# Kernel tuning notes

Measured on AMD Instinct MI355X. Metric: run time of the kernel, lower is better.

Reference implementation:

```python
import jax, jax.numpy as jnp
import numpy as np

N = 100000      # nodes
E = 1600000     # edges (before self loops)
IN_C, HID_C, OUT_C = 128, 64, 40


def setup_inputs() -> dict:
    key = jax.random.key(0)
    k = jax.random.split(key, 6)
    x = jax.random.normal(k[0], (N, IN_C), dtype=jnp.float32)
    edge_index = jax.random.randint(k[1], (2, E), 0, N, dtype=jnp.int64)
    W1 = jax.random.normal(k[2], (IN_C, HID_C), dtype=jnp.float32) * (1.0 / np.sqrt(IN_C))
    b1 = jnp.zeros((HID_C,), jnp.float32)
    W2 = jax.random.normal(k[3], (HID_C, OUT_C), dtype=jnp.float32) * (1.0 / np.sqrt(HID_C))
    b2 = jnp.zeros((OUT_C,), jnp.float32)
    beta2 = jnp.ones((), jnp.float32)  # learnable beta of prop2 (init 1.0)
    return {"x": x, "edge_index": edge_index, "W1": W1, "b1": b1,
            "W2": W2, "b2": b2, "beta2": beta2}


def _agnn_prop(x, src, dst, beta, n):
    # L2-normalize node features (F.normalize, eps=1e-12 on norm)
    xn = x * jax.lax.rsqrt(jnp.maximum(jnp.sum(x * x, axis=-1, keepdims=True), 1e-24))
    # per-edge cosine similarity scaled by beta
    alpha = beta * jnp.sum(xn[src] * xn[dst], axis=-1)           # [E']
    # scatter-softmax over edges grouped by destination node
    amax = jax.ops.segment_max(alpha, dst, num_segments=n)       # [N]
    e = jnp.exp(alpha - amax[dst])
    denom = jax.ops.segment_sum(e, dst, num_segments=n)          # [N]
    w = e / denom[dst]                                           # [E']
    # gather-weighted aggregation of (unnormalized) source features
    return jax.ops.segment_sum(x[src] * w[:, None], dst, num_segments=n)


def reference(x, edge_index, W1, b1, W2, b2, beta2):
    n = x.shape[0]
    # AGNNConv add_self_loops=True
    loops = jnp.arange(n, dtype=edge_index.dtype)
    src = jnp.concatenate([edge_index[0], loops])
    dst = jnp.concatenate([edge_index[1], loops])
    h = jax.nn.relu(x @ W1 + b1)                                 # [N, HID]
    h = _agnn_prop(h, src, dst, jnp.float32(1.0), n)             # prop1: fixed beta=1
    h = _agnn_prop(h, src, dst, beta2, n)                        # prop2: learnable beta
    logits = h @ W2 + b2                                         # [N, OUT]
    return jax.nn.log_softmax(logits, axis=1)
```

## Files before the change

### kernel.cpp

```cpp
#include <hip/hip_runtime.h>
#include <math.h>

#define INC 128
#define HID 64
#define OUTC 40
#define SHIFT 9
#define MAXB 256
#define NPB 64
#define ONB 96
#define LSW 41
#define SRCM 0x1FFFF
#define PLDS 12288

typedef _Float16 half2_t __attribute__((ext_vector_type(2)));

__device__ inline void fma4(float4& a, float s, const float4& w) {
    a.x += s * w.x; a.y += s * w.y; a.z += s * w.z; a.w += s * w.w;
}
__device__ inline unsigned pkh(float a, float b) {
    unsigned short ua = __builtin_bit_cast(unsigned short, (_Float16)a);
    unsigned short ub = __builtin_bit_cast(unsigned short, (_Float16)b);
    return (unsigned)ua | ((unsigned)ub << 16);
}
__device__ inline float fdot2_(unsigned a, unsigned b, float c) {
#if __has_builtin(__builtin_amdgcn_fdot2)
    return __builtin_amdgcn_fdot2(__builtin_bit_cast(half2_t, a),
                                  __builtin_bit_cast(half2_t, b), c, false);
#else
    half2_t ha = __builtin_bit_cast(half2_t, a);
    half2_t hb = __builtin_bit_cast(half2_t, b);
    return fmaf((float)ha[0], (float)hb[0], fmaf((float)ha[1], (float)hb[1], c));
#endif
}
__device__ inline float dot4(const uint4& a, const uint4& b) {
    float d = fdot2_(a.x, b.x, 0.f);
    d = fdot2_(a.y, b.y, d);
    d = fdot2_(a.z, b.z, d);
    d = fdot2_(a.w, b.w, d);
    return d;
}
__device__ inline void accum8(float* acc, float s, const uint4& a) {
    half2_t p;
    p = __builtin_bit_cast(half2_t, a.x); acc[0] += s * (float)p[0]; acc[1] += s * (float)p[1];
    p = __builtin_bit_cast(half2_t, a.y); acc[2] += s * (float)p[0]; acc[3] += s * (float)p[1];
    p = __builtin_bit_cast(half2_t, a.z); acc[4] += s * (float)p[0]; acc[5] += s * (float)p[1];
    p = __builtin_bit_cast(half2_t, a.w); acc[6] += s * (float)p[0]; acc[7] += s * (float)p[1];
}
__device__ inline void unpack8(float* f, const uint4& a) {
    half2_t p;
    p = __builtin_bit_cast(half2_t, a.x); f[0] = (float)p[0]; f[1] = (float)p[1];
    p = __builtin_bit_cast(half2_t, a.y); f[2] = (float)p[0]; f[3] = (float)p[1];
    p = __builtin_bit_cast(half2_t, a.z); f[4] = (float)p[0]; f[5] = (float)p[1];
    p = __builtin_bit_cast(half2_t, a.w); f[6] = (float)p[0]; f[7] = (float)p[1];
}
__device__ inline void dacc4(float4& a, unsigned xp_, const uint4& w) {
    a.x = fdot2_(xp_, w.x, a.x);
    a.y = fdot2_(xp_, w.y, a.y);
    a.z = fdot2_(xp_, w.z, a.z);
    a.w = fdot2_(xp_, w.w, a.w);
}
template<int CTRL>
__device__ inline float dppadd(float d) {
    int x = __builtin_amdgcn_update_dpp(0, __builtin_bit_cast(int, d),
                                        CTRL, 0xf, 0xf, true);
    return d + __builtin_bit_cast(float, x);
}
__device__ inline float red8(float d) {
    d = dppadd<0xB1>(d);
    d = dppadd<0x4E>(d);
    d = dppadd<0x141>(d);
    return d;
}
__device__ inline float red16(float d) {
    d = dppadd<0xB1>(d);
    d = dppadd<0x4E>(d);
    d = dppadd<0x141>(d);
    d = dppadd<0x140>(d);
    return d;
}
#define EXP2(x) __builtin_amdgcn_exp2f(x)


__global__ __launch_bounds__(256) void k_hist(const int* __restrict__ ei, int E,
                                              int* __restrict__ bucket_cnt,
                                              int* __restrict__ blk_cnt, int nbuck) {
    __shared__ int lh[MAXB];
    int tid = threadIdx.x;
    for (int i = tid; i < nbuck; i += 256) lh[i] = 0;
    __syncthreads();
    int base = blockIdx.x * 4096;
    int end = min(base + 4096, E);
    for (int e = base + tid; e < end; e += 256)
        atomicAdd(&lh[ei[E + e] >> SHIFT], 1);
    __syncthreads();
    for (int i = tid; i < nbuck; i += 256) {
        int v = lh[i];
        blk_cnt[blockIdx.x * MAXB + i] = v;
        if (v) atomicAdd(&bucket_cnt[i], v);
    }
}

__global__ __launch_bounds__(256) void k_bscan(const int* __restrict__ bucket_cnt,
                                               int* __restrict__ pair_base,
                                               int* __restrict__ pair_fill,
                                               int* __restrict__ row_ptr,
                                               int n, int E, int nbuck) {
    __shared__ int tmp[MAXB];
    int tid = threadIdx.x;
    int cnt = (tid < nbuck) ? bucket_cnt[tid] : 0;
    tmp[tid] = cnt;
    __syncthreads();
    for (int off = 1; off < 256; off <<= 1) {
        int t = (tid >= off) ? tmp[tid - off] : 0;
        __syncthreads();
        tmp[tid] += t;
        __syncthreads();
    }
    if (tid < nbuck) { int pb = tmp[tid] - cnt; pair_base[tid] = pb; pair_fill[tid] = pb; }
    if (tid == 0) row_ptr[n] = E;
}

__global__ __launch_bounds__(256) void k_bin(const int* __restrict__ ei, int E,
                                             const int* __restrict__ blk_cnt,
                                             int* __restrict__ pair_fill,
                                             unsigned* __restrict__ pairs, int nbuck) {
    __shared__ int lbase[MAXB];
    int tid = threadIdx.x;
    for (int i = tid; i < nbuck; i += 256) {
        int v = blk_cnt[blockIdx.x * MAXB + i];
        lbase[i] = v ? atomicAdd(&pair_fill[i], v) : 0;
    }
    __syncthreads();
    int base = blockIdx.x * 4096;
    int end = min(base + 4096, E);
    for (int e = base + tid; e < end; e += 256) {
        int s = ei[e], d = ei[E + e];
        int pos = atomicAdd(&lbase[d >> SHIFT], 1);
        pairs[pos] = (unsigned)s | ((unsigned)(d & ((1 << SHIFT) - 1)) << 17);
    }
}

__global__ __launch_bounds__(256) void k_build(const unsigned* __restrict__ pairs,
                                               const int* __restrict__ pair_base,
                                               const int* __restrict__ bucket_cnt,
                                               int* __restrict__ row_ptr,
                                               int* __restrict__ csr_src, int n) {
    __shared__ int cnt[1 << SHIFT];
    __shared__ int offs[1 << SHIFT];
    __shared__ int stmp[256];
    __shared__ unsigned plds[PLDS];
    int b = blockIdx.x;
    int tid = threadIdx.x;
    int nb0 = b << SHIFT;
    int W = min(n - nb0, 1 << SHIFT);
    int p0 = pair_base[b], pc = bucket_cnt[b];
    bool inl = (pc <= PLDS);

    cnt[tid] = 0; cnt[tid + 256] = 0;
    if (inl) for (int i = tid; i < pc; i += 256) plds[i] = pairs[p0 + i];
    __syncthreads();
    if (inl) {
        for (int i = tid; i < pc; i += 256) atomicAdd(&cnt[plds[i] >> 17], 1);
    } else {
        for (int i = tid; i < pc; i += 256) atomicAdd(&cnt[pairs[p0 + i] >> 17], 1);
    }
    __syncthreads();

    int i0 = 2 * tid, i1 = 2 * tid + 1;
    int s0 = (i0 < W) ? cnt[i0] : 0;
    int s1 = (i1 < W) ? cnt[i1] : 0;
    int ps = s0 + s1;
    stmp[tid] = ps;
    __syncthreads();
    for (int off = 1; off < 256; off <<= 1) {
        int t = (tid >= off) ? stmp[tid - off] : 0;
        __syncthreads();
        stmp[tid] += t;
        __syncthreads();
    }
    int excl = stmp[tid] - ps;
    if (i0 < W) { row_ptr[nb0 + i0] = p0 + excl;      offs[i0] = excl; }
    if (i1 < W) { row_ptr[nb0 + i1] = p0 + excl + s0; offs[i1] = excl + s0; }
    __syncthreads();
    if (inl) {
        for (int i = tid; i < pc; i += 256) {
            unsigned pr = plds[i];
            int pos = atomicAdd(&offs[pr >> 17], 1);
            csr_src[p0 + pos] = (int)(pr & SRCM);
        }
    } else {
        for (int i = tid; i < pc; i += 256) {
            unsigned pr = pairs[p0 + i];
            int pos = atomicAdd(&offs[pr >> 17], 1);
            csr_src[p0 + pos] = (int)(pr & SRCM);
        }
    }
}


__global__ __launch_bounds__(256, 4) void k_linear1(const float* __restrict__ x,
                                                    const float* __restrict__ W1,
                                                    const float* __restrict__ b1,
                                                    uint2* __restrict__ X1,
                                                    float* __restrict__ nrm1, int n) {
    __shared__ unsigned Wp[64 * 64];
    __shared__ unsigned xp[64 * 64];
    int tid = threadIdx.x;
    int base = blockIdx.x * NPB;

    for (int t = tid; t < 1024; t += 256) {
        int kp = t >> 4;
        int c4 = t & 15;
        float4 a = ((const float4*)W1)[(2 * kp) * 16 + c4];
        float4 b = ((const float4*)W1)[(2 * kp + 1) * 16 + c4];
        uint4 w;
        w.x = pkh(a.x, b.x); w.y = pkh(a.y, b.y);
        w.z = pkh(a.z, b.z); w.w = pkh(a.w, b.w);
        *(uint4*)&Wp[kp * 64 + c4 * 4] = w;
    }
    for (int t = tid; t < 1024; t += 256) {
        int nl = t >> 4;
        int k8 = t & 15;
        int gn = base + nl;
        float4 a, b;
        if (gn < n) {
            a = ((const float4*)x)[(size_t)gn * 32 + k8 * 2];
            b = ((const float4*)x)[(size_t)gn * 32 + k8 * 2 + 1];
        } else { a = make_float4(0,0,0,0); b = a; }
        uint4 v;
        v.x = pkh(a.x, a.y); v.y = pkh(a.z, a.w);
        v.z = pkh(b.x, b.y); v.w = pkh(b.z, b.w);
        int key = ((nl >> 2) & 3) << 2;
        *(uint4*)&xp[nl * 64 + ((k8 * 4) ^ key)] = v;
    }
    __syncthreads();

    int cg = tid & 15;
    int ng = tid >> 4;
    int n0 = ng * 4;
    const int key = (ng & 3) << 2;
    float4 acc0 = {0,0,0,0}, acc1 = {0,0,0,0}, acc2 = {0,0,0,0}, acc3 = {0,0,0,0};

    #pragma unroll 4
    for (int k4 = 0; k4 < 64; k4 += 4) {
        uint4 xq0 = *(uint4*)&xp[(n0 + 0) * 64 + (k4 ^ key)];
        uint4 xq1 = *(uint4*)&xp[(n0 + 1) * 64 + (k4 ^ key)];
        uint4 xq2 = *(uint4*)&xp[(n0 + 2) * 64 + (k4 ^ key)];
        uint4 xq3 = *(uint4*)&xp[(n0 + 3) * 64 + (k4 ^ key)];
        uint4 wq0 = *(uint4*)&Wp[(k4 + 0) * 64 + cg * 4];
        uint4 wq1 = *(uint4*)&Wp[(k4 + 1) * 64 + cg * 4];
        uint4 wq2 = *(uint4*)&Wp[(k4 + 2) * 64 + cg * 4];
        uint4 wq3 = *(uint4*)&Wp[(k4 + 3) * 64 + cg * 4];
        dacc4(acc0, xq0.x, wq0); dacc4(acc0, xq0.y, wq1); dacc4(acc0, xq0.z, wq2); dacc4(acc0, xq0.w, wq3);
        dacc4(acc1, xq1.x, wq0); dacc4(acc1, xq1.y, wq1); dacc4(acc1, xq1.z, wq2); dacc4(acc1, xq1.w, wq3);
        dacc4(acc2, xq2.x, wq0); dacc4(acc2, xq2.y, wq1); dacc4(acc2, xq2.z, wq2); dacc4(acc2, xq2.w, wq3);
        dacc4(acc3, xq3.x, wq0); dacc4(acc3, xq3.y, wq1); dacc4(acc3, xq3.z, wq2); dacc4(acc3, xq3.w, wq3);
    }

    float4 bb = ((const float4*)b1)[cg];
    float4 r[4] = {acc0, acc1, acc2, acc3};
    #pragma unroll
    for (int nl = 0; nl < 4; ++nl) {
        int node = base + n0 + nl;
        float4 v = r[nl];
        v.x = fmaxf(v.x + bb.x, 0.f); v.y = fmaxf(v.y + bb.y, 0.f);
        v.z = fmaxf(v.z + bb.z, 0.f); v.w = fmaxf(v.w + bb.w, 0.f);
        float q = v.x * v.x + v.y * v.y + v.z * v.z + v.w * v.w;
        q = red16(q);
        float rq = rsqrtf(fmaxf(q, 1e-24f));
        if (node < n) {
            X1[(size_t)node * 16 + cg] = make_uint2(pkh(v.x * rq, v.y * rq),
                                                    pkh(v.z * rq, v.w * rq));
            if (cg == 0) nrm1[node] = sqrtf(fmaxf(q, 1e-24f));
        }
    }
}


template<bool HFOUT>
__global__ __launch_bounds__(256) void k_prop(const uint4* __restrict__ X,
                                              const float* __restrict__ nrm,
                                              const int* __restrict__ row_ptr,
                                              const int* __restrict__ csr_src,
                                              const float* __restrict__ beta_ptr,
                                              uint4* __restrict__ Xout,
                                              float* __restrict__ nrm_out,
                                              float4* __restrict__ outf, int n) {
    int node = blockIdx.x * 4 + (threadIdx.x >> 6);
    if (node >= n) return;
    int lane = threadIdx.x & 63;
    int g = lane >> 3, gl = lane & 7;
    float beta = beta_ptr ? beta_ptr[0] : 1.0f;
    float b2 = beta * 1.4426950408889634f;

    uint4 hdp = X[(size_t)node * 8 + gl];
    float hdf[8]; unpack8(hdf, hdp);
    int s0 = row_ptr[node], s1 = row_ptr[node + 1];

    float ds = red8(dot4(hdp, hdp));
    float eself = EXP2(b2 * ds);
    float nd = nrm[node];
    float den0 = (g == 0) ? eself : 0.f;
    float es = (g == 0) ? eself * nd : 0.f;
    float acc[8];
    #pragma unroll
    for (int c = 0; c < 8; ++c) acc[c] = es * hdf[c];
    float den1 = 0.f;

    int j = s0;
    for (; j + 16 <= s1; j += 16) {
        int i0 = csr_src[j + g];
        int i1 = csr_src[j + 8 + g];
        uint4 a0 = X[(size_t)i0 * 8 + gl];
        uint4 a1 = X[(size_t)i1 * 8 + gl];
        float n0 = nrm[i0], n1 = nrm[i1];
        float d0 = red8(dot4(a0, hdp));
        float d1 = red8(dot4(a1, hdp));
        float e0 = EXP2(b2 * d0);
        float e1 = EXP2(b2 * d1);
        den0 += e0; den1 += e1;
        accum8(acc, e0 * n0, a0);
        accum8(acc, e1 * n1, a1);
    }
    for (; j < s1; j += 8) {
        int p0 = j + g;
        bool v0 = p0 < s1;
        int i0 = v0 ? csr_src[p0] : 0;
        uint4 a0 = X[(size_t)i0 * 8 + gl];
        float n0 = nrm[i0];
        float d0 = red8(dot4(a0, hdp));
        float e0 = v0 ? EXP2(b2 * d0) : 0.f;
        den0 += e0;
        accum8(acc, e0 * n0, a0);
    }

    float den = den0 + den1;
    #pragma unroll
    for (int c = 0; c < 8; ++c) {
        acc[c] += __shfl_xor(acc[c], 8, 64);
        acc[c] += __shfl_xor(acc[c], 16, 64);
        acc[c] += __shfl_xor(acc[c], 32, 64);
    }
    den += __shfl_xor(den, 8, 64);
    den += __shfl_xor(den, 16, 64);
    den += __shfl_xor(den, 32, 64);
    float inv = 1.0f / den;
    float o[8];
    #pragma unroll
    for (int c = 0; c < 8; ++c) o[c] = acc[c] * inv;

    if (HFOUT) {
        float q = 0.f;
        #pragma unroll
        for (int c = 0; c < 8; ++c) q += o[c] * o[c];
        q = red8(q);
        float rq = rsqrtf(fmaxf(q, 1e-24f));
        if (g == 0) {
            uint4 w;
            w.x = pkh(o[0] * rq, o[1] * rq);
            w.y = pkh(o[2] * rq, o[3] * rq);
            w.z = pkh(o[4] * rq, o[5] * rq);
            w.w = pkh(o[6] * rq, o[7] * rq);
            Xout[(size_t)node * 8 + gl] = w;
            if (gl == 0) nrm_out[node] = sqrtf(fmaxf(q, 1e-24f));
        }
    } else {
        if (g == 0) {
            outf[(size_t)node * 16 + gl * 2]     = make_float4(o[0], o[1], o[2], o[3]);
            outf[(size_t)node * 16 + gl * 2 + 1] = make_float4(o[4], o[5], o[6], o[7]);
        }
    }
}


__global__ __launch_bounds__(256) void k_out(const float* __restrict__ h,
                                             const float* __restrict__ W2,
                                             const float* __restrict__ b2,
                                             float* __restrict__ out, int n) {
    __shared__ float hs[ONB * HID];
    __shared__ float W2s[HID * OUTC];
    __shared__ float ls[ONB * LSW];
    int tid = threadIdx.x;
    int base = blockIdx.x * ONB;

    for (int i = tid; i < HID * OUTC / 4; i += 256)
        ((float4*)W2s)[i] = ((const float4*)W2)[i];
    for (int i = tid; i < ONB * 16; i += 256) {
        int nl = i >> 4, k4 = i & 15;
        int gn = base + nl;
        float4 v = (gn < n) ? ((const float4*)h)[(size_t)gn * 16 + k4]
                            : make_float4(0.f, 0.f, 0.f, 0.f);
        int swk = (k4 * 4) ^ (((nl >> 2) & 7) << 2);
        *(float4*)&hs[nl * HID + swk] = v;
    }
    __syncthreads();

    if (tid < 240) {
        int ng = tid / 10, cg = tid % 10;
        int n0 = ng * 4;
        const int sw = ((ng & 7) << 2);
        float4 acc0 = {0,0,0,0}, acc1 = {0,0,0,0}, acc2 = {0,0,0,0}, acc3 = {0,0,0,0};
        #pragma unroll 4
        for (int k = 0; k < HID; k += 4) {
            float4 w0 = *(float4*)&W2s[(k + 0) * OUTC + cg * 4];
            float4 w1 = *(float4*)&W2s[(k + 1) * OUTC + cg * 4];
            float4 w2 = *(float4*)&W2s[(k + 2) * OUTC + cg * 4];
            float4 w3 = *(float4*)&W2s[(k + 3) * OUTC + cg * 4];
            float4 x0 = *(float4*)&hs[(n0 + 0) * HID + (k ^ sw)];
            float4 x1 = *(float4*)&hs[(n0 + 1) * HID + (k ^ sw)];
            float4 x2 = *(float4*)&hs[(n0 + 2) * HID + (k ^ sw)];
            float4 x3 = *(float4*)&hs[(n0 + 3) * HID + (k ^ sw)];
            fma4(acc0, x0.x, w0); fma4(acc0, x0.y, w1); fma4(acc0, x0.z, w2); fma4(acc0, x0.w, w3);
            fma4(acc1, x1.x, w0); fma4(acc1, x1.y, w1); fma4(acc1, x1.z, w2); fma4(acc1, x1.w, w3);
            fma4(acc2, x2.x, w0); fma4(acc2, x2.y, w1); fma4(acc2, x2.z, w2); fma4(acc2, x2.w, w3);
            fma4(acc3, x3.x, w0); fma4(acc3, x3.y, w1); fma4(acc3, x3.z, w2); fma4(acc3, x3.w, w3);
        }
        float4 bb = ((const float4*)b2)[cg];
        float4 rr[4] = {acc0, acc1, acc2, acc3};
        #pragma unroll
        for (int i = 0; i < 4; ++i) {
            int lb = (n0 + i) * LSW + cg * 4;
            ls[lb + 0] = rr[i].x + bb.x;
            ls[lb + 1] = rr[i].y + bb.y;
            ls[lb + 2] = rr[i].z + bb.z;
            ls[lb + 3] = rr[i].w + bb.w;
        }
    }
    __syncthreads();

    if (tid < ONB) {
        int node = base + tid;
        if (node < n) {
            float m = -INFINITY;
            #pragma unroll
            for (int c = 0; c < OUTC; ++c) m = fmaxf(m, ls[tid * LSW + c]);
            float z = 0.f;
            #pragma unroll
            for (int c = 0; c < OUTC; ++c) z += __expf(ls[tid * LSW + c] - m);
            float lz = m + __logf(z);
            #pragma unroll
            for (int c = 0; c < OUTC; ++c)
                out[(size_t)node * OUTC + c] = ls[tid * LSW + c] - lz;
        }
    }
}


extern "C" void kernel_launch(void* const* d_in, const int* in_sizes, int n_in,
                              void* d_out, int out_size, void* d_ws, size_t ws_size,
                              hipStream_t stream) {
    const float* x   = (const float*)d_in[0];
    const int*   ei  = (const int*)d_in[1];
    const float* W1  = (const float*)d_in[2];
    const float* b1  = (const float*)d_in[3];
    const float* W2  = (const float*)d_in[4];
    const float* b2  = (const float*)d_in[5];
    const float* beta2 = (const float*)d_in[6];
    float* out = (float*)d_out;

    const int n = in_sizes[0] / INC;
    const int E = in_sizes[1] / 2;
    const int nbuck = (n + (1 << SHIFT) - 1) >> SHIFT;
    const int cgrid = (E + 4095) / 4096;

    char* p = (char*)d_ws;
    uint4* X1 = (uint4*)p;             p += (size_t)n * 8 * 16;
    uint4* X2 = (uint4*)p;             p += (size_t)n * 8 * 16;
    float* h3 = (float*)p;             p += (size_t)n * HID * 4;
    float* nrm1 = (float*)p;           p += (size_t)n * 4;
    float* nrm2 = (float*)p;           p += (size_t)n * 4;
    int* bucket_cnt  = (int*)p;        p += MAXB * 4;
    int* pair_base   = (int*)p;        p += MAXB * 4;
    int* pair_fill   = (int*)p;        p += MAXB * 4;
    int* row_ptr = (int*)p;            p += (size_t)(n + 1) * 4;
    int* csr_src = (int*)p;            p += (size_t)E * 4;
    int* blk_cnt = (int*)p;            p += (size_t)cgrid * MAXB * 4;
    unsigned* pairs = (unsigned*)h3;

    hipMemsetAsync(bucket_cnt, 0, MAXB * 4, stream);
    k_hist<<<cgrid, 256, 0, stream>>>(ei, E, bucket_cnt, blk_cnt, nbuck);
    k_bscan<<<1, 256, 0, stream>>>(bucket_cnt, pair_base, pair_fill, row_ptr, n, E, nbuck);
    k_bin<<<cgrid, 256, 0, stream>>>(ei, E, blk_cnt, pair_fill, pairs, nbuck);
    k_build<<<nbuck, 256, 0, stream>>>(pairs, pair_base, bucket_cnt, row_ptr, csr_src, n);

    k_linear1<<<(n + NPB - 1) / NPB, 256, 0, stream>>>(x, W1, b1, (uint2*)X1, nrm1, n);
    int pgrid = (n + 3) / 4;
    k_prop<true><<<pgrid, 256, 0, stream>>>(X1, nrm1, row_ptr, csr_src, nullptr,
                                            X2, nrm2, nullptr, n);
    k_prop<false><<<pgrid, 256, 0, stream>>>(X2, nrm2, row_ptr, csr_src, beta2,
                                             nullptr, nullptr, (float4*)h3, n);
    k_out<<<(n + ONB - 1) / ONB, 256, 0, stream>>>(h3, W2, b2, out, n);
}
```

Measured before the change: 195.2 us.

## Software-pipeline neighbor gathers in prop and store final prop output as fp16

The edge loop in k_prop is restructured into a single 16-wide loop that prefetches the next batch of neighbor indices, features and norms while computing the current one, with clamped indices and validity masks replacing the separate tail loop. The self-loop term is computed in closed form (exp2(beta) for a unit vector) instead of a dot product. The second propagation now writes fp16-packed features, which k_out unpacks, halving that intermediate's traffic. The risks are extra register pressure from the prefetch, redundant clamped loads in partial batches, and fp16 rounding of the unnormalized output before the final linear layer.

Result: faster. 190.5 us (-2.4%).

```diff
diff --git a/kernel.cpp b/kernel.cpp
--- a/kernel.cpp
+++ b/kernel.cpp
@@ -284,8 +284,7 @@
                                               const int* __restrict__ csr_src,
                                               const float* __restrict__ beta_ptr,
                                               uint4* __restrict__ Xout,
-                                              float* __restrict__ nrm_out,
-                                              float4* __restrict__ outf, int n) {
+                                              float* __restrict__ nrm_out, int n) {
     int node = blockIdx.x * 4 + (threadIdx.x >> 6);
     if (node >= n) return;
     int lane = threadIdx.x & 63;
@@ -294,44 +293,47 @@
     float b2 = beta * 1.4426950408889634f;
 
     uint4 hdp = X[(size_t)node * 8 + gl];
-    float hdf[8]; unpack8(hdf, hdp);
     int s0 = row_ptr[node], s1 = row_ptr[node + 1];
-
-    float ds = red8(dot4(hdp, hdp));
-    float eself = EXP2(b2 * ds);
     float nd = nrm[node];
+
+    float eself = (nd > 1.5e-12f) ? EXP2(b2) : 1.0f;
     float den0 = (g == 0) ? eself : 0.f;
     float es = (g == 0) ? eself * nd : 0.f;
-    float acc[8];
-    #pragma unroll
-    for (int c = 0; c < 8; ++c) acc[c] = es * hdf[c];
+    float acc[8] = {0, 0, 0, 0, 0, 0, 0, 0};
+    accum8(acc, es, hdp);
     float den1 = 0.f;
 
-    int j = s0;
-    for (; j + 16 <= s1; j += 16) {
-        int i0 = csr_src[j + g];
-        int i1 = csr_src[j + 8 + g];
+    if (s0 < s1) {
+        int last = s1 - 1;
+        int i0 = csr_src[min(s0 + g, last)];
+        int i1 = csr_src[min(s0 + 8 + g, last)];
         uint4 a0 = X[(size_t)i0 * 8 + gl];
         uint4 a1 = X[(size_t)i1 * 8 + gl];
         float n0 = nrm[i0], n1 = nrm[i1];
+        bool v0 = s0 + g < s1, v1 = s0 + 8 + g < s1;
+        for (int j = s0 + 16; j < s1; j += 16) {
+            int i0n = csr_src[min(j + g, last)];
+            int i1n = csr_src[min(j + 8 + g, last)];
+            uint4 a0n = X[(size_t)i0n * 8 + gl];
+            uint4 a1n = X[(size_t)i1n * 8 + gl];
+            float n0n = nrm[i0n], n1n = nrm[i1n];
+            float d0 = red8(dot4(a0, hdp));
+            float d1 = red8(dot4(a1, hdp));
+            float e0 = v0 ? EXP2(b2 * d0) : 0.f;
+            float e1 = v1 ? EXP2(b2 * d1) : 0.f;
+            den0 += e0; den1 += e1;
+            accum8(acc, e0 * n0, a0);
+            accum8(acc, e1 * n1, a1);
+            a0 = a0n; a1 = a1n; n0 = n0n; n1 = n1n;
+            v0 = j + g < s1; v1 = j + 8 + g < s1;
+        }
         float d0 = red8(dot4(a0, hdp));
         float d1 = red8(dot4(a1, hdp));
-        float e0 = EXP2(b2 * d0);
-        float e1 = EXP2(b2 * d1);
+        float e0 = v0 ? EXP2(b2 * d0) : 0.f;
+        float e1 = v1 ? EXP2(b2 * d1) : 0.f;
         den0 += e0; den1 += e1;
         accum8(acc, e0 * n0, a0);
         accum8(acc, e1 * n1, a1);
-    }
-    for (; j < s1; j += 8) {
-        int p0 = j + g;
-        bool v0 = p0 < s1;
-        int i0 = v0 ? csr_src[p0] : 0;
-        uint4 a0 = X[(size_t)i0 * 8 + gl];
-        float n0 = nrm[i0];
-        float d0 = red8(dot4(a0, hdp));
-        float e0 = v0 ? EXP2(b2 * d0) : 0.f;
-        den0 += e0;
-        accum8(acc, e0 * n0, a0);
     }
 
     float den = den0 + den1;
@@ -366,14 +368,16 @@
         }
     } else {
         if (g == 0) {
-            outf[(size_t)node * 16 + gl * 2]     = make_float4(o[0], o[1], o[2], o[3]);
-            outf[(size_t)node * 16 + gl * 2 + 1] = make_float4(o[4], o[5], o[6], o[7]);
-        }
-    }
-}
-
-
-__global__ __launch_bounds__(256) void k_out(const float* __restrict__ h,
+            uint4 w;
+            w.x = pkh(o[0], o[1]); w.y = pkh(o[2], o[3]);
+            w.z = pkh(o[4], o[5]); w.w = pkh(o[6], o[7]);
+            Xout[(size_t)node * 8 + gl] = w;
+        }
+    }
+}
+
+
+__global__ __launch_bounds__(256) void k_out(const uint4* __restrict__ Xh,
                                              const float* __restrict__ W2,
                                              const float* __restrict__ b2,
                                              float* __restrict__ out, int n) {
@@ -385,13 +389,14 @@
 
     for (int i = tid; i < HID * OUTC / 4; i += 256)
         ((float4*)W2s)[i] = ((const float4*)W2)[i];
-    for (int i = tid; i < ONB * 16; i += 256) {
-        int nl = i >> 4, k4 = i & 15;
+    for (int i = tid; i < ONB * 8; i += 256) {
+        int nl = i >> 3, k8 = i & 7;
         int gn = base + nl;
-        float4 v = (gn < n) ? ((const float4*)h)[(size_t)gn * 16 + k4]
-                            : make_float4(0.f, 0.f, 0.f, 0.f);
-        int swk = (k4 * 4) ^ (((nl >> 2) & 7) << 2);
-        *(float4*)&hs[nl * HID + swk] = v;
+        uint4 v = (gn < n) ? Xh[(size_t)gn * 8 + k8] : make_uint4(0, 0, 0, 0);
+        float f[8]; unpack8(f, v);
+        int key = ((nl >> 2) & 7) << 2;
+        *(float4*)&hs[nl * HID + ((k8 * 8) ^ key)]     = make_float4(f[0], f[1], f[2], f[3]);
+        *(float4*)&hs[nl * HID + ((k8 * 8 + 4) ^ key)] = make_float4(f[4], f[5], f[6], f[7]);
     }
     __syncthreads();
 
@@ -466,7 +471,7 @@
     char* p = (char*)d_ws;
     uint4* X1 = (uint4*)p;             p += (size_t)n * 8 * 16;
     uint4* X2 = (uint4*)p;             p += (size_t)n * 8 * 16;
-    float* h3 = (float*)p;             p += (size_t)n * HID * 4;
+    uint4* X3 = (uint4*)p;             p += (size_t)n * 8 * 16;
     float* nrm1 = (float*)p;           p += (size_t)n * 4;
     float* nrm2 = (float*)p;           p += (size_t)n * 4;
     int* bucket_cnt  = (int*)p;        p += MAXB * 4;
@@ -475,9 +480,9 @@
     int* row_ptr = (int*)p;            p += (size_t)(n + 1) * 4;
     int* csr_src = (int*)p;            p += (size_t)E * 4;
     int* blk_cnt = (int*)p;            p += (size_t)cgrid * MAXB * 4;
-    unsigned* pairs = (unsigned*)h3;
-
-    hipMemsetAsync(bucket_cnt, 0, MAXB * 4, stream);
+    unsigned* pairs = (unsigned*)X3;
+
+    (void)hipMemsetAsync(bucket_cnt, 0, MAXB * 4, stream);
     k_hist<<<cgrid, 256, 0, stream>>>(ei, E, bucket_cnt, blk_cnt, nbuck);
     k_bscan<<<1, 256, 0, stream>>>(bucket_cnt, pair_base, pair_fill, row_ptr, n, E, nbuck);
     k_bin<<<cgrid, 256, 0, stream>>>(ei, E, blk_cnt, pair_fill, pairs, nbuck);
@@ -486,8 +491,8 @@
     k_linear1<<<(n + NPB - 1) / NPB, 256, 0, stream>>>(x, W1, b1, (uint2*)X1, nrm1, n);
     int pgrid = (n + 3) / 4;
     k_prop<true><<<pgrid, 256, 0, stream>>>(X1, nrm1, row_ptr, csr_src, nullptr,
-                                            X2, nrm2, nullptr, n);
+                                            X2, nrm2, n);
     k_prop<false><<<pgrid, 256, 0, stream>>>(X2, nrm2, row_ptr, csr_src, beta2,
-                                             nullptr, nullptr, (float4*)h3, n);
-    k_out<<<(n + ONB - 1) / ONB, 256, 0, stream>>>(h3, W2, b2, out, n);
-}
+                                             X3, nullptr, n);
+    k_out<<<(n + ONB - 1) / ONB, 256, 0, stream>>>(X3, W2, b2, out, n);
+}
```
